# Kernel tuning notes

Hardware: AMD Instinct MI355X
Metric: run time of the kernel (lower is better)

## Reference

```python
import jax, jax.numpy as jnp
import numpy as np

UNITS = 1024
IN_DIM = 1024
BATCH = 4096


def setup_inputs() -> dict:
    key = jax.random.key(0)
    ks = jax.random.split(key, 11)
    C = UNITS + IN_DIM  # concat dim
    glorot = lambda k, shp: jax.random.uniform(k, shp, jnp.float32, -1.0, 1.0) * np.sqrt(6.0 / (shp[0] + shp[1]))
    return {
        "inputs": jax.random.normal(ks[0], (BATCH, IN_DIM), jnp.float32),
        "hidden_state": jax.random.normal(ks[1], (BATCH, UNITS), jnp.float32),
        "cell_state": jax.random.normal(ks[2], (BATCH, UNITS), jnp.float32),
        "W_f": glorot(ks[3], (C, UNITS)), "b_f": jnp.ones((UNITS,), jnp.float32),  # forget bias init = ones
        "W_i": glorot(ks[4], (C, UNITS)), "b_i": jnp.zeros((UNITS,), jnp.float32),
        "W_c": glorot(ks[5], (C, UNITS)), "b_c": jnp.zeros((UNITS,), jnp.float32),
        "W_o": glorot(ks[6], (C, UNITS)), "b_o": jnp.zeros((UNITS,), jnp.float32),
    }


def reference(inputs, hidden_state, cell_state, W_f, b_f, W_i, b_i, W_c, b_c, W_o, b_o):
    # concat order matches original: (hidden_state, inputs)
    x = jnp.concatenate((hidden_state, inputs), axis=1)  # [B, U+D]
    f = jax.nn.sigmoid(x @ W_f + b_f)
    i = jax.nn.sigmoid(x @ W_i + b_i)
    c_cand = jnp.tanh(x @ W_c + b_c)
    new_cell = f * cell_state + i * c_cand
    o = jax.nn.sigmoid(x @ W_o + b_o)
    new_hidden = o * jnp.tanh(new_cell)
    return (new_hidden, new_cell)
```

## Files before the change

kernel.cpp:

```cpp
#include <hip/hip_runtime.h>
#include <hip/hip_bf16.h>

#define BATCH  4096
#define UNITS  1024
#define CDIM   2048
#define NDIM   4096

typedef __attribute__((ext_vector_type(8))) short bf16x8;
typedef __attribute__((ext_vector_type(4))) short bf16x4;
typedef __attribute__((ext_vector_type(4))) float f32x4;

__device__ __forceinline__ void gload_lds16(const void* g, void* l) {
    __builtin_amdgcn_global_load_lds(
        (const __attribute__((address_space(1))) unsigned int*)g,
        (__attribute__((address_space(3))) unsigned int*)l, 16, 0, 0);
}

__device__ __forceinline__ float sigm(float x) { return 1.f / (1.f + __expf(-x)); }
__device__ __forceinline__ float tanh_fast(float x) { return 2.f / (1.f + __expf(-2.f * x)) - 1.f; }

__device__ __forceinline__ short f2bf(float f) {
    __hip_bfloat16 h = __float2bfloat16(f);
    return *reinterpret_cast<short*>(&h);
}

__global__ __launch_bounds__(256) void prep(
        const float* __restrict__ h, const float* __restrict__ in,
        const float* __restrict__ Wf, const float* __restrict__ Wi,
        const float* __restrict__ Wc, const float* __restrict__ Wo,
        __hip_bfloat16* __restrict__ x, __hip_bfloat16* __restrict__ Wt) {
    __shared__ float lds[64 * 65];
    int b = blockIdx.x, tid = threadIdx.x;
    if (b < 4096) {
        int t   = b * 256 + tid;
        int row = t >> 8;
        int c8  = (t & 255) << 3;
        const float* src = (c8 < UNITS) ? (h + (size_t)row * UNITS + c8)
                                        : (in + (size_t)row * UNITS + (c8 - UNITS));
        float4 v0 = ((const float4*)src)[0];
        float4 v1 = ((const float4*)src)[1];
        bf16x8 o;
        o[0] = f2bf(v0.x); o[1] = f2bf(v0.y); o[2] = f2bf(v0.z); o[3] = f2bf(v0.w);
        o[4] = f2bf(v1.x); o[5] = f2bf(v1.y); o[6] = f2bf(v1.z); o[7] = f2bf(v1.w);
        *(bf16x8*)(x + (size_t)row * CDIM + c8) = o;
    } else {
        int idx = b - 4096;
        int g = idx >> 9, kt = (idx >> 4) & 31, ut = idx & 15;
        const float* W = (g == 0) ? Wf : (g == 1) ? Wi : (g == 2) ? Wc : Wo;
        int k0 = kt * 64, u0 = ut * 64;
        int r16 = tid & 15, hi = tid >> 4;
#pragma unroll
        for (int it = 0; it < 4; ++it) {
            int kl = it * 16 + hi;
            float4 v = *(const float4*)&W[(size_t)(k0 + kl) * UNITS + u0 + r16 * 4];
            float* d = &lds[kl * 65 + r16 * 4];
            d[0] = v.x; d[1] = v.y; d[2] = v.z; d[3] = v.w;
        }
        __syncthreads();
#pragma unroll
        for (int it = 0; it < 4; ++it) {
            int ul = it * 16 + hi;
            int u  = u0 + ul;
            int n  = ((u >> 5) << 7) + (((u >> 4) & 1) << 6) + (g << 4) + (u & 15);
            bf16x4 o;
#pragma unroll
            for (int j = 0; j < 4; ++j) o[j] = f2bf(lds[(r16 * 4 + j) * 65 + ul]);
            *(bf16x4*)(Wt + (size_t)n * CDIM + k0 + r16 * 4) = o;
        }
    }
}

__global__ __launch_bounds__(512, 2) void gemm_lstm(
    const __hip_bfloat16* __restrict__ A,
    const __hip_bfloat16* __restrict__ Bt,
    const float* __restrict__ b_f, const float* __restrict__ b_i,
    const float* __restrict__ b_c, const float* __restrict__ b_o,
    const float* __restrict__ cell,
    float* __restrict__ out)
{
    extern __shared__ short smem[];
    const int K = CDIM;

    int bid = blockIdx.x;
    int nb  = (bid & 7) * 2 + ((bid >> 3) & 1);
    int mb  = bid >> 4;
    int m0  = mb * 256, n0 = nb * 256;

    int tid  = threadIdx.x;
    int w    = tid >> 6, lane = tid & 63;
    int wm   = w >> 2, wn2 = w & 3;
    int quad = lane >> 4, r16 = lane & 15;

    f32x4 acc[8][4];
#pragma unroll
    for (int i = 0; i < 8; ++i)
#pragma unroll
        for (int j = 0; j < 4; ++j) acc[i][j] = (f32x4){0.f, 0.f, 0.f, 0.f};

    const short* Ag0 = (const short*)A  + (size_t)(m0)       * K;
    const short* Ag1 = (const short*)A  + (size_t)(m0 + 128) * K;
    const short* Bg0 = (const short*)Bt + (size_t)(n0)       * K;
    const short* Bg1 = (const short*)Bt + (size_t)(n0 + 128) * K;

    short* lds = smem;
    unsigned SB  = (unsigned)(size_t)(__attribute__((address_space(3))) short*)smem;
    unsigned kc0 = (unsigned)((quad ^ (r16 & 7)) * 16);
    unsigned kc1 = (unsigned)(((quad + 4) ^ (r16 & 7)) * 16);
    unsigned aA  = SB + wm * 16384 + r16 * 128;
    unsigned aB  = SB + 65536 + wn2 * 8192 + r16 * 128;

    bf16x8 afX0, afX1, afX2, afX3, afY0, afY1, afY2, afY3;
    bf16x8 bfM0, bfM1, bfM2, bfM3, bfN0, bfN1, bfN2, bfN3;

#define STG(SRC, DSTOFF, KT)                                                   \
    { _Pragma("unroll")                                                        \
      for (int q_ = 0; q_ < 2; ++q_) {                                         \
          int s_ = q_ * 512 + tid;                                             \
          int row_ = s_ >> 3, cg_ = (s_ & 7) ^ (row_ & 7);                     \
          gload_lds16(SRC + (size_t)row_ * K + (KT) * 64 + cg_ * 8,            \
                      lds + (DSTOFF) + s_ * 8);                                \
      } }

#define DSR(DST, ADDR, OFFTXT)                                                 \
    asm volatile("ds_read_b128 %0, %1 " OFFTXT : "=v"(DST) : "v"(ADDR) : "memory");

#define FRAGA0(S, PB, KC) { unsigned a_ = aA + (PB) * 32768 + (KC);            \
    DSR(af##S##0, a_, "")              DSR(af##S##1, a_, "offset:2048")        \
    DSR(af##S##2, a_, "offset:4096")   DSR(af##S##3, a_, "offset:6144") }
#define FRAGA1(S, PB, KC) { unsigned a_ = aA + (PB) * 32768 + (KC);            \
    DSR(af##S##0, a_, "offset:8192")   DSR(af##S##1, a_, "offset:10240")       \
    DSR(af##S##2, a_, "offset:12288")  DSR(af##S##3, a_, "offset:14336") }
#define FRAGB(S, PB, KC) { unsigned b_ = aB + (PB) * 32768 + (KC);             \
    DSR(bf##S##0, b_, "")              DSR(bf##S##1, b_, "offset:2048")        \
    DSR(bf##S##2, b_, "offset:4096")   DSR(bf##S##3, b_, "offset:6144") }

#define MFJ(UA, BREG, IH, J)                                                   \
    acc[(IH)*4+0][J] = __builtin_amdgcn_mfma_f32_16x16x32_bf16(af##UA##0, BREG, acc[(IH)*4+0][J], 0, 0, 0); \
    acc[(IH)*4+1][J] = __builtin_amdgcn_mfma_f32_16x16x32_bf16(af##UA##1, BREG, acc[(IH)*4+1][J], 0, 0, 0); \
    acc[(IH)*4+2][J] = __builtin_amdgcn_mfma_f32_16x16x32_bf16(af##UA##2, BREG, acc[(IH)*4+2][J], 0, 0, 0); \
    acc[(IH)*4+3][J] = __builtin_amdgcn_mfma_f32_16x16x32_bf16(af##UA##3, BREG, acc[(IH)*4+3][J], 0, 0, 0);

#define PHASE(UA, UB, IH, FRAGCODE, STAGECODE, WAITCODE)                       \
    {                                                                          \
        STAGECODE;                                                             \
        WAITCODE;                                                              \
        asm volatile("s_barrier" ::: "memory");                                \
        asm volatile("s_waitcnt lgkmcnt(0)" ::: "memory");                     \
        __builtin_amdgcn_sched_barrier(0);                                     \
        FRAGCODE;                                                              \
        __builtin_amdgcn_sched_barrier(0);                                     \
        __builtin_amdgcn_s_setprio(1);                                         \
        MFJ(UA, bf##UB##0, IH, 0)                                              \
        MFJ(UA, bf##UB##1, IH, 1)                                              \
        MFJ(UA, bf##UB##2, IH, 2)                                              \
        MFJ(UA, bf##UB##3, IH, 3)                                              \
        __builtin_amdgcn_s_setprio(0);                                         \
        __builtin_amdgcn_sched_barrier(0);                                     \
        asm volatile("s_barrier" ::: "memory");                                \
    }

#define VM4 asm volatile("s_waitcnt vmcnt(4)" ::: "memory")
#define VM0 asm volatile("s_waitcnt vmcnt(0)" ::: "memory")
#define NOPX ((void)0)

    STG(Ag0, 0,     0)
    STG(Ag1, 8192,  0)
    STG(Bg0, 32768, 0)
    STG(Bg1, 40960, 0)
    STG(Bg0, 49152, 1)
    STG(Bg1, 57344, 1)
    VM4;
    asm volatile("s_barrier" ::: "memory");
    FRAGA0(X, 0, kc0)
    FRAGB(M, 0, kc0)

    for (int u = 0; u < 15; ++u) {
        int t1 = 2 * u + 1, t2 = 2 * u + 2, t3 = 2 * u + 3;
        PHASE(X, M, 0, FRAGA1(Y, 0, kc0),                   STG(Ag0, 16384, t1), NOPX)
        PHASE(Y, M, 1, FRAGA0(X, 0, kc1) FRAGB(N, 0, kc1),  STG(Ag1, 24576, t1), NOPX)
        PHASE(X, N, 0, FRAGA1(Y, 0, kc1),                   NOPX, NOPX)
        PHASE(Y, N, 1, FRAGA0(X, 1, kc0) FRAGB(M, 1, kc0),  STG(Bg0, 32768, t2) STG(Bg1, 40960, t2), VM4)
        PHASE(X, M, 0, FRAGA1(Y, 1, kc0),                   STG(Ag0, 0,     t2), NOPX)
        PHASE(Y, M, 1, FRAGA0(X, 1, kc1) FRAGB(N, 1, kc1),  STG(Ag1, 8192,  t2), NOPX)
        PHASE(X, N, 0, FRAGA1(Y, 1, kc1),                   NOPX, NOPX)
        PHASE(Y, N, 1, FRAGA0(X, 0, kc0) FRAGB(M, 0, kc0),  STG(Bg0, 49152, t3) STG(Bg1, 57344, t3), VM4)
    }
    PHASE(X, M, 0, FRAGA1(Y, 0, kc0),                   STG(Ag0, 16384, 31), NOPX)
    PHASE(Y, M, 1, FRAGA0(X, 0, kc1) FRAGB(N, 0, kc1),  STG(Ag1, 24576, 31), NOPX)
    PHASE(X, N, 0, FRAGA1(Y, 0, kc1),                   NOPX, NOPX)
    PHASE(Y, N, 1, FRAGA0(X, 1, kc0) FRAGB(M, 1, kc0),  NOPX, VM0)
    PHASE(X, M, 0, FRAGA1(Y, 1, kc0),                   NOPX, NOPX)
    PHASE(Y, M, 1, FRAGA0(X, 1, kc1) FRAGB(N, 1, kc1),  NOPX, NOPX)
    PHASE(X, N, 0, FRAGA1(Y, 1, kc1),                   NOPX, NOPX)
    PHASE(Y, N, 1, NOPX,                                NOPX, NOPX)

#undef PHASE
#undef MFJ
#undef FRAGA0
#undef FRAGA1
#undef FRAGB
#undef DSR
#undef STG
#undef VM4
#undef VM0
#undef NOPX

    int uo = nb * 64 + (wn2 >> 1) * 32 + (wn2 & 1) * 16 + r16;
    float bfv = b_f[uo], biv = b_i[uo], bcv = b_c[uo], bov = b_o[uo];
    float* out_h = out;
    float* out_c = out + (size_t)BATCH * UNITS;
#pragma unroll
    for (int i = 0; i < 8; ++i) {
#pragma unroll
        for (int rr = 0; rr < 4; ++rr) {
            int m = m0 + wm * 128 + i * 16 + quad * 4 + rr;
            float fg = sigm(acc[i][0][rr] + bfv);
            float ig = sigm(acc[i][1][rr] + biv);
            float cc = tanh_fast(acc[i][2][rr] + bcv);
            float og = sigm(acc[i][3][rr] + bov);
            float cold = cell[(size_t)m * UNITS + uo];
            float cn = fg * cold + ig * cc;
            out_h[(size_t)m * UNITS + uo] = og * tanh_fast(cn);
            out_c[(size_t)m * UNITS + uo] = cn;
        }
    }
}

extern "C" void kernel_launch(void* const* d_in, const int* in_sizes, int n_in,
                              void* d_out, int out_size, void* d_ws, size_t ws_size,
                              hipStream_t stream) {
    const float* inputs = (const float*)d_in[0];
    const float* hidden = (const float*)d_in[1];
    const float* cell   = (const float*)d_in[2];
    const float* Wf = (const float*)d_in[3];
    const float* bf_ = (const float*)d_in[4];
    const float* Wi = (const float*)d_in[5];
    const float* bi_ = (const float*)d_in[6];
    const float* Wc = (const float*)d_in[7];
    const float* bc_ = (const float*)d_in[8];
    const float* Wo = (const float*)d_in[9];
    const float* bo_ = (const float*)d_in[10];
    float* out = (float*)d_out;

    char* ws = (char*)d_ws;
    __hip_bfloat16* x  = (__hip_bfloat16*)ws;
    __hip_bfloat16* Wt = (__hip_bfloat16*)(ws + (16u << 20));

    static bool attr_set = false;
    if (!attr_set) {
        hipFuncSetAttribute(reinterpret_cast<const void*>(gemm_lstm),
                            hipFuncAttributeMaxDynamicSharedMemorySize, 131072);
        attr_set = true;
    }

    prep<<<dim3(6144), dim3(256), 0, stream>>>(hidden, inputs, Wf, Wi, Wc, Wo, x, Wt);
    gemm_lstm<<<dim3(256), dim3(512), 131072, stream>>>(
        x, Wt, bf_, bi_, bc_, bo_, cell, out);
}
```

Before: 198.5 us.

## Replace 8-phase register-prefetch pipeline with simpler 4-phase full-fragment schedule

Restructures the main GEMM loop from eight half-tile phases with double-buffered register fragments (A/B prefetched one phase ahead) into four phases. Each phase loads all eight A and four B fragments from LDS, then issues 32 MFMAs. Global-to-LDS staging of a whole K tile is issued at once, with a full vmcnt(0) wait at the end of alternate phases. This cuts barrier count and register pressure, but LDS reads are no longer overlapped with the previous phase's MFMAs, and the coarser global-load waits may expose latency.

```diff
diff --git a/kernel.cpp b/kernel.cpp
--- a/kernel.cpp
+++ b/kernel.cpp
@@ -109,9 +109,6 @@
     unsigned aA  = SB + wm * 16384 + r16 * 128;
     unsigned aB  = SB + 65536 + wn2 * 8192 + r16 * 128;
 
-    bf16x8 afX0, afX1, afX2, afX3, afY0, afY1, afY2, afY3;
-    bf16x8 bfM0, bfM1, bfM2, bfM3, bfN0, bfN1, bfN2, bfN3;
-
 #define STG(SRC, DSTOFF, KT)                                                   \
     { _Pragma("unroll")                                                        \
       for (int q_ = 0; q_ < 2; ++q_) {                                         \
@@ -124,42 +121,43 @@
 #define DSR(DST, ADDR, OFFTXT)                                                 \
     asm volatile("ds_read_b128 %0, %1 " OFFTXT : "=v"(DST) : "v"(ADDR) : "memory");
 
-#define FRAGA0(S, PB, KC) { unsigned a_ = aA + (PB) * 32768 + (KC);            \
-    DSR(af##S##0, a_, "")              DSR(af##S##1, a_, "offset:2048")        \
-    DSR(af##S##2, a_, "offset:4096")   DSR(af##S##3, a_, "offset:6144") }
-#define FRAGA1(S, PB, KC) { unsigned a_ = aA + (PB) * 32768 + (KC);            \
-    DSR(af##S##0, a_, "offset:8192")   DSR(af##S##1, a_, "offset:10240")       \
-    DSR(af##S##2, a_, "offset:12288")  DSR(af##S##3, a_, "offset:14336") }
-#define FRAGB(S, PB, KC) { unsigned b_ = aB + (PB) * 32768 + (KC);             \
-    DSR(bf##S##0, b_, "")              DSR(bf##S##1, b_, "offset:2048")        \
-    DSR(bf##S##2, b_, "offset:4096")   DSR(bf##S##3, b_, "offset:6144") }
-
-#define MFJ(UA, BREG, IH, J)                                                   \
-    acc[(IH)*4+0][J] = __builtin_amdgcn_mfma_f32_16x16x32_bf16(af##UA##0, BREG, acc[(IH)*4+0][J], 0, 0, 0); \
-    acc[(IH)*4+1][J] = __builtin_amdgcn_mfma_f32_16x16x32_bf16(af##UA##1, BREG, acc[(IH)*4+1][J], 0, 0, 0); \
-    acc[(IH)*4+2][J] = __builtin_amdgcn_mfma_f32_16x16x32_bf16(af##UA##2, BREG, acc[(IH)*4+2][J], 0, 0, 0); \
-    acc[(IH)*4+3][J] = __builtin_amdgcn_mfma_f32_16x16x32_bf16(af##UA##3, BREG, acc[(IH)*4+3][J], 0, 0, 0);
-
-#define PHASE(UA, UB, IH, FRAGCODE, STAGECODE, WAITCODE)                       \
+#define MFJ8(BREG, J)                                                          \
+    acc[0][J] = __builtin_amdgcn_mfma_f32_16x16x32_bf16(af0_, BREG, acc[0][J], 0, 0, 0); \
+    acc[1][J] = __builtin_amdgcn_mfma_f32_16x16x32_bf16(af1_, BREG, acc[1][J], 0, 0, 0); \
+    acc[2][J] = __builtin_amdgcn_mfma_f32_16x16x32_bf16(af2_, BREG, acc[2][J], 0, 0, 0); \
+    acc[3][J] = __builtin_amdgcn_mfma_f32_16x16x32_bf16(af3_, BREG, acc[3][J], 0, 0, 0); \
+    acc[4][J] = __builtin_amdgcn_mfma_f32_16x16x32_bf16(af4_, BREG, acc[4][J], 0, 0, 0); \
+    acc[5][J] = __builtin_amdgcn_mfma_f32_16x16x32_bf16(af5_, BREG, acc[5][J], 0, 0, 0); \
+    acc[6][J] = __builtin_amdgcn_mfma_f32_16x16x32_bf16(af6_, BREG, acc[6][J], 0, 0, 0); \
+    acc[7][J] = __builtin_amdgcn_mfma_f32_16x16x32_bf16(af7_, BREG, acc[7][J], 0, 0, 0);
+
+#define MPHASE(P, KC, STAGECODE, WAITCODE)                                     \
     {                                                                          \
+        unsigned adA_ = aA + (P) * 32768 + (KC);                               \
+        unsigned adB_ = aB + (P) * 32768 + (KC);                               \
+        bf16x8 af0_, af1_, af2_, af3_, af4_, af5_, af6_, af7_;                 \
+        bf16x8 bf0_, bf1_, bf2_, bf3_;                                         \
+        DSR(af0_, adA_, "")               DSR(af1_, adA_, "offset:2048")       \
+        DSR(af2_, adA_, "offset:4096")    DSR(af3_, adA_, "offset:6144")       \
+        DSR(af4_, adA_, "offset:8192")    DSR(af5_, adA_, "offset:10240")      \
+        DSR(af6_, adA_, "offset:12288")   DSR(af7_, adA_, "offset:14336")      \
+        DSR(bf0_, adB_, "")               DSR(bf1_, adB_, "offset:2048")       \
+        DSR(bf2_, adB_, "offset:4096")    DSR(bf3_, adB_, "offset:6144")       \
         STAGECODE;                                                             \
-        WAITCODE;                                                              \
         asm volatile("s_barrier" ::: "memory");                                \
         asm volatile("s_waitcnt lgkmcnt(0)" ::: "memory");                     \
         __builtin_amdgcn_sched_barrier(0);                                     \
-        FRAGCODE;                                                              \
-        __builtin_amdgcn_sched_barrier(0);                                     \
         __builtin_amdgcn_s_setprio(1);                                         \
-        MFJ(UA, bf##UB##0, IH, 0)                                              \
-        MFJ(UA, bf##UB##1, IH, 1)                                              \
-        MFJ(UA, bf##UB##2, IH, 2)                                              \
-        MFJ(UA, bf##UB##3, IH, 3)                                              \
+        MFJ8(bf0_, 0)                                                          \
+        MFJ8(bf1_, 1)                                                          \
+        MFJ8(bf2_, 2)                                                          \
+        MFJ8(bf3_, 3)                                                          \
         __builtin_amdgcn_s_setprio(0);                                         \
         __builtin_amdgcn_sched_barrier(0);                                     \
+        WAITCODE;                                                              \
         asm volatile("s_barrier" ::: "memory");                                \
     }
 
-#define VM4 asm volatile("s_waitcnt vmcnt(4)" ::: "memory")
 #define VM0 asm volatile("s_waitcnt vmcnt(0)" ::: "memory")
 #define NOPX ((void)0)
 
@@ -167,41 +165,28 @@
     STG(Ag1, 8192,  0)
     STG(Bg0, 32768, 0)
     STG(Bg1, 40960, 0)
-    STG(Bg0, 49152, 1)
-    STG(Bg1, 57344, 1)
-    VM4;
+    VM0;
     asm volatile("s_barrier" ::: "memory");
-    FRAGA0(X, 0, kc0)
-    FRAGB(M, 0, kc0)
 
     for (int u = 0; u < 15; ++u) {
-        int t1 = 2 * u + 1, t2 = 2 * u + 2, t3 = 2 * u + 3;
-        PHASE(X, M, 0, FRAGA1(Y, 0, kc0),                   STG(Ag0, 16384, t1), NOPX)
-        PHASE(Y, M, 1, FRAGA0(X, 0, kc1) FRAGB(N, 0, kc1),  STG(Ag1, 24576, t1), NOPX)
-        PHASE(X, N, 0, FRAGA1(Y, 0, kc1),                   NOPX, NOPX)
-        PHASE(Y, N, 1, FRAGA0(X, 1, kc0) FRAGB(M, 1, kc0),  STG(Bg0, 32768, t2) STG(Bg1, 40960, t2), VM4)
-        PHASE(X, M, 0, FRAGA1(Y, 1, kc0),                   STG(Ag0, 0,     t2), NOPX)
-        PHASE(Y, M, 1, FRAGA0(X, 1, kc1) FRAGB(N, 1, kc1),  STG(Ag1, 8192,  t2), NOPX)
-        PHASE(X, N, 0, FRAGA1(Y, 1, kc1),                   NOPX, NOPX)
-        PHASE(Y, N, 1, FRAGA0(X, 0, kc0) FRAGB(M, 0, kc0),  STG(Bg0, 49152, t3) STG(Bg1, 57344, t3), VM4)
-    }
-    PHASE(X, M, 0, FRAGA1(Y, 0, kc0),                   STG(Ag0, 16384, 31), NOPX)
-    PHASE(Y, M, 1, FRAGA0(X, 0, kc1) FRAGB(N, 0, kc1),  STG(Ag1, 24576, 31), NOPX)
-    PHASE(X, N, 0, FRAGA1(Y, 0, kc1),                   NOPX, NOPX)
-    PHASE(Y, N, 1, FRAGA0(X, 1, kc0) FRAGB(M, 1, kc0),  NOPX, VM0)
-    PHASE(X, M, 0, FRAGA1(Y, 1, kc0),                   NOPX, NOPX)
-    PHASE(Y, M, 1, FRAGA0(X, 1, kc1) FRAGB(N, 1, kc1),  NOPX, NOPX)
-    PHASE(X, N, 0, FRAGA1(Y, 1, kc1),                   NOPX, NOPX)
-    PHASE(Y, N, 1, NOPX,                                NOPX, NOPX)
-
-#undef PHASE
-#undef MFJ
-#undef FRAGA0
-#undef FRAGA1
-#undef FRAGB
+        int t1 = 2 * u + 1, t2 = 2 * u + 2;
+        MPHASE(0, kc0, STG(Ag0, 16384, t1) STG(Ag1, 24576, t1)
+                       STG(Bg0, 49152, t1) STG(Bg1, 57344, t1), NOPX)
+        MPHASE(0, kc1, NOPX, VM0)
+        MPHASE(1, kc0, STG(Ag0, 0,     t2) STG(Ag1, 8192,  t2)
+                       STG(Bg0, 32768, t2) STG(Bg1, 40960, t2), NOPX)
+        MPHASE(1, kc1, NOPX, VM0)
+    }
+    MPHASE(0, kc0, STG(Ag0, 16384, 31) STG(Ag1, 24576, 31)
+                   STG(Bg0, 49152, 31) STG(Bg1, 57344, 31), NOPX)
+    MPHASE(0, kc1, NOPX, VM0)
+    MPHASE(1, kc0, NOPX, NOPX)
+    MPHASE(1, kc1, NOPX, NOPX)
+
+#undef MPHASE
+#undef MFJ8
 #undef DSR
 #undef STG
-#undef VM4
 #undef VM0
 #undef NOPX
 
```

After: 204.1 us. +2.8%, slower.
